# Kernel tuning notes

Hardware: AMD Instinct MI355X
Metric: run time of the kernel (lower is better)

Reference implementation:

```python
import jax, jax.numpy as jnp
import numpy as np

B, N, D = 8, 2048, 512

def setup_inputs() -> dict:
    key = jax.random.key(0)
    k1, k2, k3, k4, k5 = jax.random.split(key, 5)
    s = 1.0 / np.sqrt(D)
    return {
        "x": jax.random.normal(k1, (B, N, D), dtype=jnp.float32),
        "w_qkv": jax.random.normal(k2, (D, 3 * D), dtype=jnp.float32) * s,
        "b_qkv": jax.random.normal(k3, (3 * D,), dtype=jnp.float32) * 0.01,
        "w_fc": jax.random.normal(k4, (D, D), dtype=jnp.float32) * s,
        "b_fc": jax.random.normal(k5, (D,), dtype=jnp.float32) * 0.01,
    }

def reference(x, w_qkv, b_qkv, w_fc, b_fc):
    scale = 1.0 / (x.shape[-1] ** 0.5)
    qkv = x @ w_qkv + b_qkv                      # [B, N, 3D]
    q, k, v = jnp.split(qkv, 3, axis=-1)         # each [B, N, D]
    attn = jnp.einsum("bnd,bmd->bnm", q, k) * scale
    attn = jax.nn.softmax(attn, axis=-1)
    out = jnp.einsum("bnm,bmd->bnd", attn, v)
    return out @ w_fc + b_fc + x
```

## Files before the change

kernel.cpp:

```cpp
#include <hip/hip_runtime.h>
#include <stdint.h>

typedef unsigned short u16;
typedef unsigned int u32;
typedef __attribute__((ext_vector_type(8))) short short8;
typedef __attribute__((ext_vector_type(4))) float f32x4;
typedef __attribute__((ext_vector_type(8))) unsigned short u16x8;
typedef __attribute__((ext_vector_type(4))) float float4_t;

__device__ __forceinline__ float b2f(u16 u) { return __uint_as_float(((u32)u) << 16); }
__device__ __forceinline__ u16 f2b(float f) {
  u32 u = __float_as_uint(f);
  u += 0x7fffu + ((u >> 16) & 1u);
  return (u16)(u >> 16);
}

typedef const __attribute__((address_space(1))) void* gas_t;
typedef __attribute__((address_space(3))) void* las_t;
__device__ __forceinline__ void gl_lds16(const void* g, void* l) {
  __builtin_amdgcn_global_load_lds((gas_t)(uintptr_t)g, (las_t)(u32)(uintptr_t)l, 16, 0, 0);
}
__device__ __forceinline__ void barrier_pin() {
  __builtin_amdgcn_sched_barrier(0);
  __builtin_amdgcn_s_barrier();
  __builtin_amdgcn_sched_barrier(0);
}
__device__ __forceinline__ void lgkm0_pin() {
  asm volatile("s_waitcnt lgkmcnt(0)" ::: "memory");
  __builtin_amdgcn_sched_barrier(0);
}

__global__ __launch_bounds__(256) void cvt_f2b_kernel(const float* __restrict__ src,
                                                      u16* __restrict__ dst, long n) {
  long i = ((long)blockIdx.x * 256 + threadIdx.x) * 8;
  if (i >= n) return;
  float4_t v0 = *(const float4_t*)(src + i);
  float4_t v1 = *(const float4_t*)(src + i + 4);
  u16x8 o;
#pragma unroll
  for (int j = 0; j < 4; ++j) { o[j] = f2b(v0[j]); o[4 + j] = f2b(v1[j]); }
  *(u16x8*)(dst + i) = o;
}

__global__ __launch_bounds__(256) void tr_cvt(const float* __restrict__ src,
                                              u16* __restrict__ dst, int R, int C) {
  __shared__ float t[32][33];
  const int bx = blockIdx.x * 32;
  const int by = blockIdx.y * 32;
  const int tx = threadIdx.x & 31, ty = threadIdx.x >> 5;
#pragma unroll
  for (int i = 0; i < 32; i += 8)
    t[ty + i][tx] = src[(long)(by + ty + i) * C + bx + tx];
  __syncthreads();
#pragma unroll
  for (int i = 0; i < 32; i += 8)
    dst[(long)(bx + ty + i) * R + by + tx] = f2b(t[tx][ty + i]);
}

__global__ __launch_bounds__(256) void tr_v(const u16* __restrict__ qkv, u16* __restrict__ vt) {
  __shared__ u16 t[32][33];
  const int b = blockIdx.z;
  const int r0 = blockIdx.x * 32;
  const int d0 = blockIdx.y * 32;
  const int tx = threadIdx.x & 31, ty = threadIdx.x >> 5;
#pragma unroll
  for (int i = 0; i < 32; i += 8)
    t[ty + i][tx] = qkv[((long)b * 2048 + r0 + ty + i) * 1536 + 1024 + d0 + tx];
  __syncthreads();
#pragma unroll
  for (int i = 0; i < 32; i += 8)
    vt[((long)b * 512 + d0 + ty + i) * 2048 + r0 + tx] = t[tx][ty + i];
}

template <bool OUT_F32, bool BIAS, bool RES, bool EXP_EPI, bool ROWSUM_DIV>
__global__ __launch_bounds__(512, 4)
void gemm128(const u16* __restrict__ A, const u16* __restrict__ Bt, void* __restrict__ Cv,
             const float* __restrict__ bias, const float* __restrict__ res,
             int K, int lda, int ldb, int ldc,
             long aStride, long bStride, long cStride, float alpha) {
  __shared__ u16 As[2][128 * 64];
  __shared__ u16 Bs[2][128 * 64];
  __shared__ float lsum[ROWSUM_DIV ? 128 : 1];
  const int tid = threadIdx.x;
  const int wid = tid >> 6, lane = tid & 63;
  const int wr = wid >> 2, wc = wid & 3;
  const int lr = lane & 15, lg = lane >> 4;

  const int gx = gridDim.x, gy = gridDim.y;
  int id = (blockIdx.z * gy + blockIdx.y) * gx + blockIdx.x;
  const int nwg = gx * gy * gridDim.z;
  id = (id & 7) * (nwg >> 3) + (id >> 3);
  const int bxi = id % gx;
  const int t2 = id / gx;
  const int byi = t2 % gy;
  const long z = t2 / gy;

  A += z * aStride;
  Bt += z * bStride;
  const int by = byi * 128;
  const int bx = bxi * 128;

  f32x4 acc[4][2] = {};
  f32x4 acc_l[4] = {};
  short8 ah[4][2], bh[2][2];
  short8 ones;
#pragma unroll
  for (int j = 0; j < 8; ++j) ones[j] = (short)0x3F80;

  const int w8l = wid * 8 + (lane >> 3);
  const int scol_src = ((lane & 7) ^ (lane >> 3)) * 8;
  const int scol_lin = (lane & 7) * 8;
  const int nT = K >> 6;
  const int sx = lane & 7;

  auto stage = [&](int kt) {
    const int bb = kt & 1;
    const long kc = (long)kt * 64 + scol_src;
#pragma unroll
    for (int r = 0; r < 2; ++r) {
      const int row = r * 64 + w8l;
      gl_lds16(A + (long)(by + row) * lda + kc, &As[bb][row * 64 + scol_lin]);
    }
#pragma unroll
    for (int r = 0; r < 2; ++r) {
      const int row = r * 64 + w8l;
      gl_lds16(Bt + (long)(bx + row) * ldb + kc, &Bs[bb][row * 64 + scol_lin]);
    }
  };

  stage(0);
  asm volatile("s_waitcnt vmcnt(0)" ::: "memory");
  barrier_pin();

  for (int T = 0; T < nT; ++T) {
    const int bb = T & 1;
    const bool more = (T + 1) < nT;
    if (more) stage(T + 1);
#pragma unroll
    for (int mi = 0; mi < 4; ++mi)
#pragma unroll
      for (int ks = 0; ks < 2; ++ks)
        ah[mi][ks] = *(const short8*)&As[bb][(wr * 64 + mi * 16 + lr) * 64 +
                                             (((ks * 4 + lg) ^ sx) * 8)];
#pragma unroll
    for (int n = 0; n < 2; ++n)
#pragma unroll
      for (int ks = 0; ks < 2; ++ks)
        bh[n][ks] = *(const short8*)&Bs[bb][(wc * 32 + n * 16 + lr) * 64 +
                                            (((ks * 4 + lg) ^ sx) * 8)];
    lgkm0_pin();
    __builtin_amdgcn_s_setprio(1);
#pragma unroll
    for (int mi = 0; mi < 4; ++mi)
#pragma unroll
      for (int n = 0; n < 2; ++n)
#pragma unroll
        for (int ks = 0; ks < 2; ++ks)
          acc[mi][n] = __builtin_amdgcn_mfma_f32_16x16x32_bf16(
              ah[mi][ks], bh[n][ks], acc[mi][n], 0, 0, 0);
    if constexpr (ROWSUM_DIV) {
      if (wc == 0) {
#pragma unroll
        for (int mi = 0; mi < 4; ++mi)
#pragma unroll
          for (int ks = 0; ks < 2; ++ks)
            acc_l[mi] = __builtin_amdgcn_mfma_f32_16x16x32_bf16(
                ah[mi][ks], ones, acc_l[mi], 0, 0, 0);
      }
    }
    __builtin_amdgcn_s_setprio(0);
    if (more) asm volatile("s_waitcnt vmcnt(0)" ::: "memory");
    barrier_pin();
  }

  if constexpr (ROWSUM_DIV) {
    if (wc == 0 && lr == 0) {
#pragma unroll
      for (int mi = 0; mi < 4; ++mi)
#pragma unroll
        for (int j = 0; j < 4; ++j)
          lsum[wr * 64 + mi * 16 + lg * 4 + j] = acc_l[mi][j];
    }
    __syncthreads();
  }

  if constexpr (EXP_EPI) {
    u16* C = (u16*)Cv + z * cStride;
#pragma unroll
    for (int mi = 0; mi < 4; ++mi)
#pragma unroll
      for (int ni = 0; ni < 2; ++ni)
#pragma unroll
        for (int j = 0; j < 4; ++j) {
          const long row = by + wr * 64 + mi * 16 + lg * 4 + j;
          const int col = bx + wc * 32 + ni * 16 + lr;
          C[row * (long)ldc + col] = f2b(__expf(acc[mi][ni][j] * alpha));
        }
  } else if constexpr (OUT_F32) {
    float* C = (float*)Cv + z * cStride;
#pragma unroll
    for (int mi = 0; mi < 4; ++mi)
#pragma unroll
      for (int ni = 0; ni < 2; ++ni)
#pragma unroll
        for (int j = 0; j < 4; ++j) {
          const long row = by + wr * 64 + mi * 16 + lg * 4 + j;
          const int col = bx + wc * 32 + ni * 16 + lr;
          float v = acc[mi][ni][j] * alpha;
          if (BIAS) v += bias[col];
          if (RES) v += res[row * (long)ldc + col];
          C[row * (long)ldc + col] = v;
        }
  } else {
    u16* C = (u16*)Cv + z * cStride;
#pragma unroll
    for (int mi = 0; mi < 4; ++mi)
#pragma unroll
      for (int j = 0; j < 4; ++j) {
        float invl = 1.0f;
        if constexpr (ROWSUM_DIV) invl = 1.0f / lsum[wr * 64 + mi * 16 + lg * 4 + j];
#pragma unroll
        for (int ni = 0; ni < 2; ++ni) {
          const long row = by + wr * 64 + mi * 16 + lg * 4 + j;
          const int col = bx + wc * 32 + ni * 16 + lr;
          float v = acc[mi][ni][j] * alpha;
          if constexpr (ROWSUM_DIV) v *= invl;
          if (BIAS) v += bias[col];
          C[row * (long)ldc + col] = f2b(v);
        }
      }
  }
}

extern "C" void kernel_launch(void* const* d_in, const int* in_sizes, int n_in,
                              void* d_out, int out_size, void* d_ws, size_t ws_size,
                              hipStream_t stream) {
  const float* x = (const float*)d_in[0];
  const float* w_qkv = (const float*)d_in[1];
  const float* b_qkv = (const float*)d_in[2];
  const float* w_fc = (const float*)d_in[3];
  const float* b_fc = (const float*)d_in[4];
  float* out = (float*)d_out;

  char* ws = (char*)d_ws;
  const long MT = 16384;
  u16* xb = (u16*)(ws);
  u16* wqkvT = (u16*)(ws + 16777216);
  u16* wfcT = (u16*)(ws + 18350080);
  u16* qkv = (u16*)(ws + 18874368);
  u16* vt = (u16*)(ws + 69206016);
  u16* S = (u16*)(ws + 85983232);
  u16* attn = xb;

  cvt_f2b_kernel<<<4096, 256, 0, stream>>>(x, xb, MT * 512);
  tr_cvt<<<dim3(48, 16), 256, 0, stream>>>(w_qkv, wqkvT, 512, 1536);
  tr_cvt<<<dim3(16, 16), 256, 0, stream>>>(w_fc, wfcT, 512, 512);

  gemm128<false, true, false, false, false><<<dim3(12, 128, 1), 512, 0, stream>>>(
      xb, wqkvT, qkv, b_qkv, nullptr,
      512, 512, 512, 1536, 0, 0, 0, 1.0f);

  tr_v<<<dim3(64, 16, 8), 256, 0, stream>>>(qkv, vt);

  gemm128<false, false, false, true, false><<<dim3(16, 16, 8), 512, 0, stream>>>(
      qkv, qkv + 512, S, nullptr, nullptr,
      512, 1536, 1536, 2048,
      (long)2048 * 1536, (long)2048 * 1536, (long)2048 * 2048, 0.04419417382415922f);

  gemm128<false, false, false, false, true><<<dim3(4, 16, 8), 512, 0, stream>>>(
      S, vt, attn, nullptr, nullptr,
      2048, 2048, 2048, 512,
      (long)2048 * 2048, (long)512 * 2048, (long)2048 * 512, 1.0f);

  gemm128<true, true, true, false, false><<<dim3(4, 128, 1), 512, 0, stream>>>(
      attn, wfcT, out, b_fc, x,
      512, 512, 512, 512, 0, 0, 0, 1.0f);
}
```

Baseline: 163.6 us.

## Use 256x128 GEMM tiles with K=32 stages for QKV, QK^T and output GEMMs

Introduces a new GEMM kernel with 256x128 output tiles, a 32-wide K step and a 4x4 MFMA accumulator per wave. It is used for the QKV projection, the QK^T score GEMM and the output projection. The PV GEMM with the row-sum division moves to its own specialized 128x128 kernel. Larger tiles raise arithmetic intensity and halve block count, at the cost of more registers per wave and twice as many K iterations with barriers.

```diff
diff --git a/kernel.cpp b/kernel.cpp
--- a/kernel.cpp
+++ b/kernel.cpp
@@ -72,18 +72,17 @@
     vt[((long)b * 512 + d0 + ty + i) * 2048 + r0 + tx] = t[tx][ty + i];
 }
 
-template <bool OUT_F32, bool BIAS, bool RES, bool EXP_EPI, bool ROWSUM_DIV>
+template <bool OUT_F32, bool BIAS, bool RES, bool EXP_EPI>
 __global__ __launch_bounds__(512, 4)
-void gemm128(const u16* __restrict__ A, const u16* __restrict__ Bt, void* __restrict__ Cv,
-             const float* __restrict__ bias, const float* __restrict__ res,
-             int K, int lda, int ldb, int ldc,
-             long aStride, long bStride, long cStride, float alpha) {
-  __shared__ u16 As[2][128 * 64];
-  __shared__ u16 Bs[2][128 * 64];
-  __shared__ float lsum[ROWSUM_DIV ? 128 : 1];
+void gemm256n(const u16* __restrict__ A, const u16* __restrict__ Bt, void* __restrict__ Cv,
+              const float* __restrict__ bias, const float* __restrict__ res,
+              int K, int lda, int ldb, int ldc,
+              long aStride, long bStride, long cStride, float alpha) {
+  __shared__ u16 As[2][256 * 32];
+  __shared__ u16 Bs[2][128 * 32];
   const int tid = threadIdx.x;
   const int wid = tid >> 6, lane = tid & 63;
-  const int wr = wid >> 2, wc = wid & 3;
+  const int wr = wid >> 1, wc = wid & 1;
   const int lr = lane & 15, lg = lane >> 4;
 
   const int gx = gridDim.x, gy = gridDim.y;
@@ -97,35 +96,30 @@
 
   A += z * aStride;
   Bt += z * bStride;
-  const int by = byi * 128;
+  const int by = byi * 256;
   const int bx = bxi * 128;
 
-  f32x4 acc[4][2] = {};
-  f32x4 acc_l[4] = {};
-  short8 ah[4][2], bh[2][2];
-  short8 ones;
-#pragma unroll
-  for (int j = 0; j < 8; ++j) ones[j] = (short)0x3F80;
-
-  const int w8l = wid * 8 + (lane >> 3);
-  const int scol_src = ((lane & 7) ^ (lane >> 3)) * 8;
-  const int scol_lin = (lane & 7) * 8;
-  const int nT = K >> 6;
-  const int sx = lane & 7;
+  f32x4 acc[4][4] = {};
+  short8 ah[4], bh[4];
+
+  const int th_row = tid >> 2;
+  const int slot_lin = (tid & 3) * 8;
+  const int slot_src = (((tid & 3) ^ ((tid >> 2) & 3)) * 8);
+  const int nT = K >> 5;
+  const int sx = lr & 3;
+
+  const u16* Ag0 = A + (long)(by + th_row) * lda + slot_src;
+  const u16* Ag1 = Ag0 + (long)128 * lda;
+  const u16* Bg  = Bt + (long)(bx + th_row) * ldb + slot_src;
+  const int dA = th_row * 32 + slot_lin;
+  const int dB = dA;
 
   auto stage = [&](int kt) {
     const int bb = kt & 1;
-    const long kc = (long)kt * 64 + scol_src;
-#pragma unroll
-    for (int r = 0; r < 2; ++r) {
-      const int row = r * 64 + w8l;
-      gl_lds16(A + (long)(by + row) * lda + kc, &As[bb][row * 64 + scol_lin]);
-    }
-#pragma unroll
-    for (int r = 0; r < 2; ++r) {
-      const int row = r * 64 + w8l;
-      gl_lds16(Bt + (long)(bx + row) * ldb + kc, &Bs[bb][row * 64 + scol_lin]);
-    }
+    const long ko = (long)kt * 32;
+    gl_lds16(Ag0 + ko, &As[bb][dA]);
+    gl_lds16(Ag1 + ko, &As[bb][dA + 128 * 32]);
+    gl_lds16(Bg + ko, &Bs[bb][dB]);
   };
 
   stage(0);
@@ -138,62 +132,33 @@
     if (more) stage(T + 1);
 #pragma unroll
     for (int mi = 0; mi < 4; ++mi)
-#pragma unroll
-      for (int ks = 0; ks < 2; ++ks)
-        ah[mi][ks] = *(const short8*)&As[bb][(wr * 64 + mi * 16 + lr) * 64 +
-                                             (((ks * 4 + lg) ^ sx) * 8)];
-#pragma unroll
-    for (int n = 0; n < 2; ++n)
-#pragma unroll
-      for (int ks = 0; ks < 2; ++ks)
-        bh[n][ks] = *(const short8*)&Bs[bb][(wc * 32 + n * 16 + lr) * 64 +
-                                            (((ks * 4 + lg) ^ sx) * 8)];
+      ah[mi] = *(const short8*)&As[bb][(wr * 64 + mi * 16 + lr) * 32 + ((lg ^ sx) * 8)];
+#pragma unroll
+    for (int ni = 0; ni < 4; ++ni)
+      bh[ni] = *(const short8*)&Bs[bb][(wc * 64 + ni * 16 + lr) * 32 + ((lg ^ sx) * 8)];
     lgkm0_pin();
     __builtin_amdgcn_s_setprio(1);
 #pragma unroll
     for (int mi = 0; mi < 4; ++mi)
 #pragma unroll
-      for (int n = 0; n < 2; ++n)
-#pragma unroll
-        for (int ks = 0; ks < 2; ++ks)
-          acc[mi][n] = __builtin_amdgcn_mfma_f32_16x16x32_bf16(
-              ah[mi][ks], bh[n][ks], acc[mi][n], 0, 0, 0);
-    if constexpr (ROWSUM_DIV) {
-      if (wc == 0) {
-#pragma unroll
-        for (int mi = 0; mi < 4; ++mi)
-#pragma unroll
-          for (int ks = 0; ks < 2; ++ks)
-            acc_l[mi] = __builtin_amdgcn_mfma_f32_16x16x32_bf16(
-                ah[mi][ks], ones, acc_l[mi], 0, 0, 0);
-      }
-    }
+      for (int ni = 0; ni < 4; ++ni)
+        acc[mi][ni] = __builtin_amdgcn_mfma_f32_16x16x32_bf16(
+            ah[mi], bh[ni], acc[mi][ni], 0, 0, 0);
     __builtin_amdgcn_s_setprio(0);
     if (more) asm volatile("s_waitcnt vmcnt(0)" ::: "memory");
     barrier_pin();
   }
 
-  if constexpr (ROWSUM_DIV) {
-    if (wc == 0 && lr == 0) {
-#pragma unroll
-      for (int mi = 0; mi < 4; ++mi)
-#pragma unroll
-        for (int j = 0; j < 4; ++j)
-          lsum[wr * 64 + mi * 16 + lg * 4 + j] = acc_l[mi][j];
-    }
-    __syncthreads();
-  }
-
   if constexpr (EXP_EPI) {
     u16* C = (u16*)Cv + z * cStride;
 #pragma unroll
     for (int mi = 0; mi < 4; ++mi)
 #pragma unroll
-      for (int ni = 0; ni < 2; ++ni)
+      for (int ni = 0; ni < 4; ++ni)
 #pragma unroll
         for (int j = 0; j < 4; ++j) {
           const long row = by + wr * 64 + mi * 16 + lg * 4 + j;
-          const int col = bx + wc * 32 + ni * 16 + lr;
+          const int col = bx + wc * 64 + ni * 16 + lr;
           C[row * (long)ldc + col] = f2b(__expf(acc[mi][ni][j] * alpha));
         }
   } else if constexpr (OUT_F32) {
@@ -201,11 +166,11 @@
 #pragma unroll
     for (int mi = 0; mi < 4; ++mi)
 #pragma unroll
-      for (int ni = 0; ni < 2; ++ni)
+      for (int ni = 0; ni < 4; ++ni)
 #pragma unroll
         for (int j = 0; j < 4; ++j) {
           const long row = by + wr * 64 + mi * 16 + lg * 4 + j;
-          const int col = bx + wc * 32 + ni * 16 + lr;
+          const int col = bx + wc * 64 + ni * 16 + lr;
           float v = acc[mi][ni][j] * alpha;
           if (BIAS) v += bias[col];
           if (RES) v += res[row * (long)ldc + col];
@@ -216,20 +181,137 @@
 #pragma unroll
     for (int mi = 0; mi < 4; ++mi)
 #pragma unroll
-      for (int j = 0; j < 4; ++j) {
-        float invl = 1.0f;
-        if constexpr (ROWSUM_DIV) invl = 1.0f / lsum[wr * 64 + mi * 16 + lg * 4 + j];
-#pragma unroll
-        for (int ni = 0; ni < 2; ++ni) {
+      for (int ni = 0; ni < 4; ++ni)
+#pragma unroll
+        for (int j = 0; j < 4; ++j) {
           const long row = by + wr * 64 + mi * 16 + lg * 4 + j;
-          const int col = bx + wc * 32 + ni * 16 + lr;
+          const int col = bx + wc * 64 + ni * 16 + lr;
           float v = acc[mi][ni][j] * alpha;
-          if constexpr (ROWSUM_DIV) v *= invl;
           if (BIAS) v += bias[col];
           C[row * (long)ldc + col] = f2b(v);
         }
+  }
+}
+
+__global__ __launch_bounds__(512, 4)
+void gemm128_pv(const u16* __restrict__ A, const u16* __restrict__ Bt, u16* __restrict__ Cv,
+                int K, int lda, int ldb, int ldc,
+                long aStride, long bStride, long cStride) {
+  __shared__ u16 As[2][128 * 64];
+  __shared__ u16 Bs[2][128 * 64];
+  __shared__ float lsum[128];
+  const int tid = threadIdx.x;
+  const int wid = tid >> 6, lane = tid & 63;
+  const int wr = wid >> 2, wc = wid & 3;
+  const int lr = lane & 15, lg = lane >> 4;
+
+  const int gx = gridDim.x, gy = gridDim.y;
+  int id = (blockIdx.z * gy + blockIdx.y) * gx + blockIdx.x;
+  const int nwg = gx * gy * gridDim.z;
+  id = (id & 7) * (nwg >> 3) + (id >> 3);
+  const int bxi = id % gx;
+  const int t2 = id / gx;
+  const int byi = t2 % gy;
+  const long z = t2 / gy;
+
+  A += z * aStride;
+  Bt += z * bStride;
+  const int by = byi * 128;
+  const int bx = bxi * 128;
+
+  f32x4 acc[4][2] = {};
+  f32x4 acc_l[4] = {};
+  short8 ah[4][2], bh[2][2];
+  short8 ones;
+#pragma unroll
+  for (int j = 0; j < 8; ++j) ones[j] = (short)0x3F80;
+
+  const int w8l = wid * 8 + (lane >> 3);
+  const int scol_src = ((lane & 7) ^ (lane >> 3)) * 8;
+  const int scol_lin = (lane & 7) * 8;
+  const int nT = K >> 6;
+  const int sx = lane & 7;
+
+  auto stage = [&](int kt) {
+    const int bb = kt & 1;
+    const long kc = (long)kt * 64 + scol_src;
+#pragma unroll
+    for (int r = 0; r < 2; ++r) {
+      const int row = r * 64 + w8l;
+      gl_lds16(A + (long)(by + row) * lda + kc, &As[bb][row * 64 + scol_lin]);
+    }
+#pragma unroll
+    for (int r = 0; r < 2; ++r) {
+      const int row = r * 64 + w8l;
+      gl_lds16(Bt + (long)(bx + row) * ldb + kc, &Bs[bb][row * 64 + scol_lin]);
+    }
+  };
+
+  stage(0);
+  asm volatile("s_waitcnt vmcnt(0)" ::: "memory");
+  barrier_pin();
+
+  for (int T = 0; T < nT; ++T) {
+    const int bb = T & 1;
+    const bool more = (T + 1) < nT;
+    if (more) stage(T + 1);
+#pragma unroll
+    for (int mi = 0; mi < 4; ++mi)
+#pragma unroll
+      for (int ks = 0; ks < 2; ++ks)
+        ah[mi][ks] = *(const short8*)&As[bb][(wr * 64 + mi * 16 + lr) * 64 +
+                                             (((ks * 4 + lg) ^ sx) * 8)];
+#pragma unroll
+    for (int n = 0; n < 2; ++n)
+#pragma unroll
+      for (int ks = 0; ks < 2; ++ks)
+        bh[n][ks] = *(const short8*)&Bs[bb][(wc * 32 + n * 16 + lr) * 64 +
+                                            (((ks * 4 + lg) ^ sx) * 8)];
+    lgkm0_pin();
+    __builtin_amdgcn_s_setprio(1);
+#pragma unroll
+    for (int mi = 0; mi < 4; ++mi)
+#pragma unroll
+      for (int n = 0; n < 2; ++n)
+#pragma unroll
+        for (int ks = 0; ks < 2; ++ks)
+          acc[mi][n] = __builtin_amdgcn_mfma_f32_16x16x32_bf16(
+              ah[mi][ks], bh[n][ks], acc[mi][n], 0, 0, 0);
+    if (wc == 0) {
+#pragma unroll
+      for (int mi = 0; mi < 4; ++mi)
+#pragma unroll
+        for (int ks = 0; ks < 2; ++ks)
+          acc_l[mi] = __builtin_amdgcn_mfma_f32_16x16x32_bf16(
+              ah[mi][ks], ones, acc_l[mi], 0, 0, 0);
+    }
+    __builtin_amdgcn_s_setprio(0);
+    if (more) asm volatile("s_waitcnt vmcnt(0)" ::: "memory");
+    barrier_pin();
+  }
+
+  if (wc == 0 && lr == 0) {
+#pragma unroll
+    for (int mi = 0; mi < 4; ++mi)
+#pragma unroll
+      for (int j = 0; j < 4; ++j)
+        lsum[wr * 64 + mi * 16 + lg * 4 + j] = acc_l[mi][j];
+  }
+  __syncthreads();
+
+  u16* C = Cv + z * cStride;
+#pragma unroll
+  for (int mi = 0; mi < 4; ++mi)
+#pragma unroll
+    for (int j = 0; j < 4; ++j) {
+      const float invl = 1.0f / lsum[wr * 64 + mi * 16 + lg * 4 + j];
+#pragma unroll
+      for (int ni = 0; ni < 2; ++ni) {
+        const long row = by + wr * 64 + mi * 16 + lg * 4 + j;
+        const int col = bx + wc * 32 + ni * 16 + lr;
+        C[row * (long)ldc + col] = f2b(acc[mi][ni][j] * invl);
       }
-  }
+    }
 }
 
 extern "C" void kernel_launch(void* const* d_in, const int* in_sizes, int n_in,
@@ -256,23 +338,23 @@
   tr_cvt<<<dim3(48, 16), 256, 0, stream>>>(w_qkv, wqkvT, 512, 1536);
   tr_cvt<<<dim3(16, 16), 256, 0, stream>>>(w_fc, wfcT, 512, 512);
 
-  gemm128<false, true, false, false, false><<<dim3(12, 128, 1), 512, 0, stream>>>(
+  gemm256n<false, true, false, false><<<dim3(12, 64, 1), 512, 0, stream>>>(
       xb, wqkvT, qkv, b_qkv, nullptr,
       512, 512, 512, 1536, 0, 0, 0, 1.0f);
 
   tr_v<<<dim3(64, 16, 8), 256, 0, stream>>>(qkv, vt);
 
-  gemm128<false, false, false, true, false><<<dim3(16, 16, 8), 512, 0, stream>>>(
+  gemm256n<false, false, false, true><<<dim3(16, 8, 8), 512, 0, stream>>>(
       qkv, qkv + 512, S, nullptr, nullptr,
       512, 1536, 1536, 2048,
       (long)2048 * 1536, (long)2048 * 1536, (long)2048 * 2048, 0.04419417382415922f);
 
-  gemm128<false, false, false, false, true><<<dim3(4, 16, 8), 512, 0, stream>>>(
-      S, vt, attn, nullptr, nullptr,
+  gemm128_pv<<<dim3(4, 16, 8), 512, 0, stream>>>(
+      S, vt, attn,
       2048, 2048, 2048, 512,
-      (long)2048 * 2048, (long)512 * 2048, (long)2048 * 512, 1.0f);
-
-  gemm128<true, true, true, false, false><<<dim3(4, 128, 1), 512, 0, stream>>>(
+      (long)2048 * 2048, (long)512 * 2048, (long)2048 * 512);
+
+  gemm256n<true, true, true, false><<<dim3(4, 64, 1), 512, 0, stream>>>(
       attn, wfcT, out, b_fc, x,
       512, 512, 512, 512, 0, 0, 0, 1.0f);
 }
```

New measurement: 170.2 us. 1.04x slower.

## Switch GEMM to triple-buffered K=32 tiles with two-stage-ahead prefetch

Applied to the files above, without the earlier changes.

The shared GEMM kernel now uses three LDS buffers of 128x32 instead of two of 128x64, and prefetches two K-tiles ahead. It waits with vmcnt(2) so one load batch stays in flight during compute. Each iteration does half the MFMAs, so it needs twice as many barriers per K. The swizzle is adapted to the 32-wide rows. LDS use per block drops, which may allow more occupancy, but the barrier overhead per unit of work goes up.

```diff
diff --git a/kernel.cpp b/kernel.cpp
--- a/kernel.cpp
+++ b/kernel.cpp
@@ -74,12 +74,12 @@
 
 template <bool OUT_F32, bool BIAS, bool RES, bool EXP_EPI, bool ROWSUM_DIV>
 __global__ __launch_bounds__(512, 4)
-void gemm128(const u16* __restrict__ A, const u16* __restrict__ Bt, void* __restrict__ Cv,
-             const float* __restrict__ bias, const float* __restrict__ res,
-             int K, int lda, int ldb, int ldc,
-             long aStride, long bStride, long cStride, float alpha) {
-  __shared__ u16 As[2][128 * 64];
-  __shared__ u16 Bs[2][128 * 64];
+void gemm128t(const u16* __restrict__ A, const u16* __restrict__ Bt, void* __restrict__ Cv,
+              const float* __restrict__ bias, const float* __restrict__ res,
+              int K, int lda, int ldb, int ldc,
+              long aStride, long bStride, long cStride, float alpha) {
+  __shared__ u16 As[3][128 * 32];
+  __shared__ u16 Bs[3][128 * 32];
   __shared__ float lsum[ROWSUM_DIV ? 128 : 1];
   const int tid = threadIdx.x;
   const int wid = tid >> 6, lane = tid & 63;
@@ -102,74 +102,61 @@
 
   f32x4 acc[4][2] = {};
   f32x4 acc_l[4] = {};
-  short8 ah[4][2], bh[2][2];
+  short8 ah[4], bh[2];
   short8 ones;
 #pragma unroll
   for (int j = 0; j < 8; ++j) ones[j] = (short)0x3F80;
 
-  const int w8l = wid * 8 + (lane >> 3);
-  const int scol_src = ((lane & 7) ^ (lane >> 3)) * 8;
-  const int scol_lin = (lane & 7) * 8;
-  const int nT = K >> 6;
-  const int sx = lane & 7;
+  const int th_row = tid >> 2;
+  const int slot_lin = (tid & 3) * 8;
+  const int slot_src = (((tid & 3) ^ ((tid >> 3) & 3)) * 8);
+  const int nT = K >> 5;
+  const int sxk = (lr >> 1) & 3;
+
+  const u16* Ag = A + (long)(by + th_row) * lda + slot_src;
+  const u16* Bg = Bt + (long)(bx + th_row) * ldb + slot_src;
+  const int dL = th_row * 32 + slot_lin;
 
   auto stage = [&](int kt) {
-    const int bb = kt & 1;
-    const long kc = (long)kt * 64 + scol_src;
-#pragma unroll
-    for (int r = 0; r < 2; ++r) {
-      const int row = r * 64 + w8l;
-      gl_lds16(A + (long)(by + row) * lda + kc, &As[bb][row * 64 + scol_lin]);
-    }
-#pragma unroll
-    for (int r = 0; r < 2; ++r) {
-      const int row = r * 64 + w8l;
-      gl_lds16(Bt + (long)(bx + row) * ldb + kc, &Bs[bb][row * 64 + scol_lin]);
-    }
+    int bb = kt % 3;
+    const long ko = (long)kt * 32;
+    gl_lds16(Ag + ko, &As[bb][dL]);
+    gl_lds16(Bg + ko, &Bs[bb][dL]);
   };
 
   stage(0);
-  asm volatile("s_waitcnt vmcnt(0)" ::: "memory");
+  stage(1);
+  asm volatile("s_waitcnt vmcnt(2)" ::: "memory");
   barrier_pin();
 
   for (int T = 0; T < nT; ++T) {
-    const int bb = T & 1;
-    const bool more = (T + 1) < nT;
-    if (more) stage(T + 1);
-#pragma unroll
-    for (int mi = 0; mi < 4; ++mi)
-#pragma unroll
-      for (int ks = 0; ks < 2; ++ks)
-        ah[mi][ks] = *(const short8*)&As[bb][(wr * 64 + mi * 16 + lr) * 64 +
-                                             (((ks * 4 + lg) ^ sx) * 8)];
+    const int bb = T % 3;
+    if (T + 2 < nT) stage(T + 2);
+#pragma unroll
+    for (int mi = 0; mi < 4; ++mi)
+      ah[mi] = *(const short8*)&As[bb][(wr * 64 + mi * 16 + lr) * 32 + ((lg ^ sxk) * 8)];
 #pragma unroll
     for (int n = 0; n < 2; ++n)
-#pragma unroll
-      for (int ks = 0; ks < 2; ++ks)
-        bh[n][ks] = *(const short8*)&Bs[bb][(wc * 32 + n * 16 + lr) * 64 +
-                                            (((ks * 4 + lg) ^ sx) * 8)];
+      bh[n] = *(const short8*)&Bs[bb][(wc * 32 + n * 16 + lr) * 32 + ((lg ^ sxk) * 8)];
     lgkm0_pin();
     __builtin_amdgcn_s_setprio(1);
 #pragma unroll
     for (int mi = 0; mi < 4; ++mi)
 #pragma unroll
       for (int n = 0; n < 2; ++n)
-#pragma unroll
-        for (int ks = 0; ks < 2; ++ks)
-          acc[mi][n] = __builtin_amdgcn_mfma_f32_16x16x32_bf16(
-              ah[mi][ks], bh[n][ks], acc[mi][n], 0, 0, 0);
+        acc[mi][n] = __builtin_amdgcn_mfma_f32_16x16x32_bf16(
+            ah[mi], bh[n], acc[mi][n], 0, 0, 0);
     if constexpr (ROWSUM_DIV) {
       if (wc == 0) {
 #pragma unroll
         for (int mi = 0; mi < 4; ++mi)
-#pragma unroll
-          for (int ks = 0; ks < 2; ++ks)
-            acc_l[mi] = __builtin_amdgcn_mfma_f32_16x16x32_bf16(
-                ah[mi][ks], ones, acc_l[mi], 0, 0, 0);
+          acc_l[mi] = __builtin_amdgcn_mfma_f32_16x16x32_bf16(
+              ah[mi], ones, acc_l[mi], 0, 0, 0);
       }
     }
     __builtin_amdgcn_s_setprio(0);
-    if (more) asm volatile("s_waitcnt vmcnt(0)" ::: "memory");
+    if (T + 2 < nT)      asm volatile("s_waitcnt vmcnt(2)" ::: "memory");
+    else if (T + 1 < nT) asm volatile("s_waitcnt vmcnt(0)" ::: "memory");
     barrier_pin();
   }
 
@@ -256,23 +243,23 @@
   tr_cvt<<<dim3(48, 16), 256, 0, stream>>>(w_qkv, wqkvT, 512, 1536);
   tr_cvt<<<dim3(16, 16), 256, 0, stream>>>(w_fc, wfcT, 512, 512);
 
-  gemm128<false, true, false, false, false><<<dim3(12, 128, 1), 512, 0, stream>>>(
+  gemm128t<false, true, false, false, false><<<dim3(12, 128, 1), 512, 0, stream>>>(
       xb, wqkvT, qkv, b_qkv, nullptr,
       512, 512, 512, 1536, 0, 0, 0, 1.0f);
 
   tr_v<<<dim3(64, 16, 8), 256, 0, stream>>>(qkv, vt);
 
-  gemm128<false, false, false, true, false><<<dim3(16, 16, 8), 512, 0, stream>>>(
+  gemm128t<false, false, false, true, false><<<dim3(16, 16, 8), 512, 0, stream>>>(
       qkv, qkv + 512, S, nullptr, nullptr,
       512, 1536, 1536, 2048,
       (long)2048 * 1536, (long)2048 * 1536, (long)2048 * 2048, 0.04419417382415922f);
 
-  gemm128<false, false, false, false, true><<<dim3(4, 16, 8), 512, 0, stream>>>(
+  gemm128t<false, false, false, false, true><<<dim3(4, 16, 8), 512, 0, stream>>>(
       S, vt, attn, nullptr, nullptr,
       2048, 2048, 2048, 512,
       (long)2048 * 2048, (long)512 * 2048, (long)2048 * 512, 1.0f);
 
-  gemm128<true, true, true, false, false><<<dim3(4, 128, 1), 512, 0, stream>>>(
+  gemm128t<true, true, true, false, false><<<dim3(4, 128, 1), 512, 0, stream>>>(
       attn, wfcT, out, b_fc, x,
       512, 512, 512, 512, 0, 0, 0, 1.0f);
 }
```

Result: slower. 173.7 us (+6.2%).
